# Performance work log

Hardware: AMD Instinct MI355X
Metric: run time of the kernel (lower is better)

Reference implementation:

```python
import jax, jax.numpy as jnp
import numpy as np

D_MODEL = 64
N_RULES = 4
C_DIM = 128
B, T = 32, 8192
LN_EPS = 1e-5
POSSIBLE_STEPS = np.array([2.0, 3.0, 4.0, 5.0, 6.0, 7.0, 8.0], dtype=np.float32)


def setup_inputs() -> dict:
    key = jax.random.key(0)
    ks = jax.random.split(key, 24)
    s = 0.05
    d, h, c = D_MODEL, 2 * D_MODEL, C_DIM
    inp = {
        "cells_state": jax.random.normal(ks[0], (B, T, d), jnp.float32),
        "c_state": jax.random.normal(ks[1], (c,), jnp.float32),
        # n_rules stacked 2-layer rule MLPs: (3d -> 2d, GELU) -> (2d -> d, Tanh)
        "rule_w1": jax.random.normal(ks[2], (N_RULES, 3 * d, h), jnp.float32) * s,
        "rule_b1": jnp.zeros((N_RULES, h), jnp.float32),
        "rule_w2": jax.random.normal(ks[3], (N_RULES, h, d), jnp.float32) * s,
        "rule_b2": jnp.zeros((N_RULES, d), jnp.float32),
        # c_selector: c -> 64 -> n_rules
        "sel_w1": jax.random.normal(ks[4], (c, 64), jnp.float32) * s,
        "sel_b1": jnp.zeros((64,), jnp.float32),
        "sel_w2": jax.random.normal(ks[5], (64, N_RULES), jnp.float32) * s,
        "sel_b2": jnp.zeros((N_RULES,), jnp.float32),
        # c_steps_logits: c -> 32 -> 7
        "st_w1": jax.random.normal(ks[6], (c, 32), jnp.float32) * s,
        "st_b1": jnp.zeros((32,), jnp.float32),
        "st_w2": jax.random.normal(ks[7], (32, 7), jnp.float32) * s,
        "st_b2": jnp.zeros((7,), jnp.float32),
        # c_residual: c -> 32 -> 1, Sigmoid
        "res_w1": jax.random.normal(ks[8], (c, 32), jnp.float32) * s,
        "res_b1": jnp.zeros((32,), jnp.float32),
        "res_w2": jax.random.normal(ks[9], (32, 1), jnp.float32) * s,
        "res_b2": jnp.zeros((1,), jnp.float32),
        # LayerNorm affine
        "ln_g": jnp.ones((d,), jnp.float32),
        "ln_b": jnp.zeros((d,), jnp.float32),
    }
    return inp


def _mlp2(x, w1, b1, w2, b2):
    h = jax.nn.gelu(x @ w1 + b1, approximate=False)
    return h @ w2 + b2


def reference(cells_state, c_state, rule_w1, rule_b1, rule_w2, rule_b2,
              sel_w1, sel_b1, sel_w2, sel_b2, st_w1, st_b1, st_w2, st_b2,
              res_w1, res_b1, res_w2, res_b2, ln_g, ln_b):
    # consciousness-derived controls
    rule_weights = jax.nn.softmax(_mlp2(c_state, sel_w1, sel_b1, sel_w2, sel_b2))  # [n_rules]
    steps_weights = jax.nn.softmax(_mlp2(c_state, st_w1, st_b1, st_w2, st_b2))     # [7]
    n_evolve_soft = jnp.sum(steps_weights * jnp.asarray(POSSIBLE_STEPS))
    # host-side step count (matches torch .item() rounding); concrete, not traced
    n_evolve = max(2, min(8, int(float(n_evolve_soft) + 0.5)))
    alpha = 0.1 + 0.8 * jax.nn.sigmoid(_mlp2(c_state, res_w1, res_b1, res_w2, res_b2))[0]

    cells = cells_state
    for _ in range(n_evolve):
        left = jnp.roll(cells, 1, axis=1)
        right = jnp.roll(cells, -1, axis=1)
        rule_input = jnp.concatenate([cells, left, right], axis=-1)            # [B,T,3d]
        h = jax.nn.gelu(jnp.einsum('btk,rkh->rbth', rule_input, rule_w1)
                        + rule_b1[:, None, None, :], approximate=False)        # [r,B,T,2d]
        out = jnp.tanh(jnp.einsum('rbth,rhd->rbtd', h, rule_w2)
                       + rule_b2[:, None, None, :])                            # [r,B,T,d]
        new_cells = jnp.einsum('r,rbtd->btd', rule_weights, out)
        cells = alpha * cells + (1.0 - alpha) * new_cells

    mu = jnp.mean(cells, axis=-1, keepdims=True)
    var = jnp.mean(jnp.square(cells - mu), axis=-1, keepdims=True)
    normed = (cells - mu) * jax.lax.rsqrt(var + LN_EPS) * ln_g + ln_b
    return normed
```

## Files before the change

### kernel.cpp

```cpp
#include <hip/hip_runtime.h>
#include <cmath>

#define D 64
#define HD 128
#define K1 192
#define TT 8192
#define BBATCH 32
#define RULES 4

typedef _Float16 f16x8 __attribute__((ext_vector_type(8)));
typedef _Float16 f16x4 __attribute__((ext_vector_type(4)));
typedef float f32x4 __attribute__((ext_vector_type(4)));

__device__ __forceinline__ float gelu_exact(float x) {
    return 0.5f * x * (1.0f + erff(x * 0.70710678118654752f));
}

__device__ __forceinline__ float fast_rcp(float x) { return __builtin_amdgcn_rcpf(x); }
__device__ __forceinline__ float fast_exp2(float x) { return __builtin_amdgcn_exp2f(x); }

__device__ __forceinline__ float gelu_tanh(float x) {
    float x2 = x * x;
    float t = x * fmaf(x2, -0.10294443f, -2.30220820f);
    return x * fast_rcp(1.0f + fast_exp2(t));
}
__device__ __forceinline__ float fast_tanh(float x) {
    float e = fast_exp2(x * 2.8853900817779268f);
    return 1.0f - 2.0f * fast_rcp(e + 1.0f);
}

__device__ __forceinline__ f16x4 cvt4_rne(float a, float b, float c, float d) {
    f16x4 r;
    r[0] = (_Float16)a; r[1] = (_Float16)b;
    r[2] = (_Float16)c; r[3] = (_Float16)d;
    return r;
}

__global__ __launch_bounds__(256) void prep_control_kernel(
    const float* __restrict__ rule_w1, const float* __restrict__ rule_w2,
    _Float16* __restrict__ w1b, _Float16* __restrict__ w2b,
    const float* __restrict__ c_state,
    const float* __restrict__ sel_w1, const float* __restrict__ sel_b1,
    const float* __restrict__ sel_w2, const float* __restrict__ sel_b2,
    const float* __restrict__ st_w1,  const float* __restrict__ st_b1,
    const float* __restrict__ st_w2,  const float* __restrict__ st_b2,
    const float* __restrict__ res_w1, const float* __restrict__ res_b1,
    const float* __restrict__ res_w2, const float* __restrict__ res_b2,
    float* __restrict__ ctrl)
{
    if (blockIdx.x < 64) {
        int t = blockIdx.x * 256 + threadIdx.x;
        if (t < 12288) {
            int lane = t & 63;
            int x = t >> 6;
            int htile = x & 31;
            int ks = x >> 5;
            int r = htile >> 3;
            int h128 = (htile & 7) * 16 + (lane & 15);
            int kbase = ks * 32 + (lane >> 4) * 8;
            f16x8 v;
#pragma unroll
            for (int j = 0; j < 8; ++j)
                v[j] = (_Float16)rule_w1[((size_t)r * K1 + kbase + j) * HD + h128];
            ((f16x8*)w1b)[(ks * 32 + htile) * 64 + lane] = v;
        } else if (t < 12288 + 4096) {
            int u = t - 12288;
            int lane = u & 63;
            int mt = (u >> 6) & 3;
            int ks2 = (u >> 8) & 3;
            int r = u >> 10;
            int kbase = ks2 * 32 + (lane >> 4) * 8;
            int d = mt * 16 + (lane & 15);
            f16x8 v;
#pragma unroll
            for (int j = 0; j < 8; ++j)
                v[j] = (_Float16)rule_w2[((size_t)r * HD + kbase + j) * D + d];
            ((f16x8*)w2b)[((r * 4 + ks2) * 4 + mt) * 64 + lane] = v;
        }
        return;
    }

    __shared__ float cs[128];
    __shared__ float h1s[64], h2s[32], h3s[32];
    __shared__ float lg[12];
    int l = threadIdx.x;
    if (l < 64) { cs[l] = c_state[l]; cs[l + 64] = c_state[l + 64]; }
    __syncthreads();
    if (l < 64) {
        float a = sel_b1[l];
        for (int k = 0; k < 128; ++k) a += cs[k] * sel_w1[k * 64 + l];
        h1s[l] = gelu_exact(a);
    }
    if (l < 32) {
        float a = st_b1[l];
        for (int k = 0; k < 128; ++k) a += cs[k] * st_w1[k * 32 + l];
        h2s[l] = gelu_exact(a);
        float a2 = res_b1[l];
        for (int k = 0; k < 128; ++k) a2 += cs[k] * res_w1[k * 32 + l];
        h3s[l] = gelu_exact(a2);
    }
    __syncthreads();
    if (l < 4) {
        float a = sel_b2[l];
        for (int j = 0; j < 64; ++j) a += h1s[j] * sel_w2[j * 4 + l];
        lg[l] = a;
    }
    if (l >= 8 && l < 15) {
        int s = l - 8;
        float a = st_b2[s];
        for (int j = 0; j < 32; ++j) a += h2s[j] * st_w2[j * 7 + s];
        lg[4 + s] = a;
    }
    if (l == 32) {
        float a = res_b2[0];
        for (int j = 0; j < 32; ++j) a += h3s[j] * res_w2[j];
        lg[11] = a;
    }
    __syncthreads();
    if (l == 0) {
        float m = fmaxf(fmaxf(lg[0], lg[1]), fmaxf(lg[2], lg[3]));
        float e0 = expf(lg[0] - m), e1 = expf(lg[1] - m);
        float e2 = expf(lg[2] - m), e3 = expf(lg[3] - m);
        float s = e0 + e1 + e2 + e3;
        ctrl[0] = e0 / s; ctrl[1] = e1 / s; ctrl[2] = e2 / s; ctrl[3] = e3 / s;
        float m2 = lg[4];
        for (int i = 1; i < 7; ++i) m2 = fmaxf(m2, lg[4 + i]);
        float ss = 0.f, es[7];
        for (int i = 0; i < 7; ++i) { es[i] = expf(lg[4 + i] - m2); ss += es[i]; }
        float nsoft = 0.f;
        for (int i = 0; i < 7; ++i) nsoft += (es[i] / ss) * (float)(i + 2);
        int n = (int)(nsoft + 0.5f);
        n = n < 2 ? 2 : (n > 8 ? 8 : n);
        float alpha = 0.1f + 0.8f / (1.0f + expf(-lg[11]));
        ctrl[4] = alpha;
        ctrl[5] = (float)n;
    }
}

__device__ __forceinline__ void evolve_tile(
    int tile, const float* __restrict__ src, float* __restrict__ dst,
    const _Float16* __restrict__ w1b, const _Float16* __restrict__ w2b,
    const float* __restrict__ b1, const float* __restrict__ b2,
    const float* __restrict__ ln_g, const float* __restrict__ ln_b,
    float* __restrict__ fin, bool last, float alpha, float beta, float rwr,
    _Float16* cellsL, _Float16 (*arena)[64 * 136])
{
    int b = tile >> 7;
    int t0 = (tile & 127) << 6;
    const float* srcb = src + (size_t)b * TT * D;

    int tid = threadIdx.x;
    for (int idx = tid; idx < 66 * 16; idx += 256) {
        int row = idx >> 4;
        int c4 = (idx & 15) << 2;
        int tok = (t0 - 1 + row) & (TT - 1);
        f32x4 v = *(const f32x4*)(srcb + (size_t)tok * D + c4);
        *(f16x4*)&cellsL[row * 72 + c4] = cvt4_rne(v[0], v[1], v[2], v[3]);
    }
    __syncthreads();

    int wave = tid >> 6;
    int lane = tid & 63;
    int lrow = lane & 15;
    int lgrp = lane >> 4;
    int r = wave;

    const f16x8* w1v = (const f16x8*)w1b;
    const f16x8* w2v = (const f16x8*)w2b;
    _Float16* hb = &arena[wave][0];

    f32x4 acc1[8][4];
#pragma unroll
    for (int ht = 0; ht < 8; ++ht)
#pragma unroll
        for (int nt = 0; nt < 4; ++nt)
            acc1[ht][nt] = (f32x4){0.f, 0.f, 0.f, 0.f};

#pragma unroll
    for (int ks = 0; ks < 6; ++ks) {
        int k0 = ks * 32 + lgrp * 8;
        int seg = k0 >> 6;
        int kk = k0 & 63;
        int drow = (seg == 0) ? 1 : ((seg == 1) ? 0 : 2);
        f16x8 a_[4];
#pragma unroll
        for (int nt = 0; nt < 4; ++nt)
            a_[nt] = *(const f16x8*)&cellsL[(nt * 16 + lrow + drow) * 72 + kk];
#pragma unroll
        for (int ht = 0; ht < 8; ++ht) {
            f16x8 wf = w1v[(ks * 32 + r * 8 + ht) * 64 + lane];
#pragma unroll
            for (int nt = 0; nt < 4; ++nt)
                acc1[ht][nt] = __builtin_amdgcn_mfma_f32_16x16x32_f16(wf, a_[nt], acc1[ht][nt], 0, 0, 0);
        }
    }

#pragma unroll
    for (int ht = 0; ht < 8; ++ht) {
        f32x4 b1v = *(const f32x4*)&b1[r * HD + ht * 16 + lgrp * 4];
#pragma unroll
        for (int nt = 0; nt < 4; ++nt) {
            float g0 = gelu_tanh(acc1[ht][nt][0] + b1v[0]);
            float g1 = gelu_tanh(acc1[ht][nt][1] + b1v[1]);
            float g2 = gelu_tanh(acc1[ht][nt][2] + b1v[2]);
            float g3 = gelu_tanh(acc1[ht][nt][3] + b1v[3]);
            *(f16x4*)&hb[(nt * 16 + lrow) * 136 + ht * 16 + lgrp * 4]
                = cvt4_rne(g0, g1, g2, g3);
        }
    }

    f32x4 acc2[4][4];
#pragma unroll
    for (int mt = 0; mt < 4; ++mt)
#pragma unroll
        for (int nt = 0; nt < 4; ++nt)
            acc2[mt][nt] = (f32x4){0.f, 0.f, 0.f, 0.f};

#pragma unroll
    for (int ks2 = 0; ks2 < 4; ++ks2) {
        f16x8 a2[4];
#pragma unroll
        for (int nt = 0; nt < 4; ++nt)
            a2[nt] = *(const f16x8*)&hb[(nt * 16 + lrow) * 136 + ks2 * 32 + lgrp * 8];
#pragma unroll
        for (int mt = 0; mt < 4; ++mt) {
            f16x8 bw = w2v[((r * 4 + ks2) * 4 + mt) * 64 + lane];
#pragma unroll
            for (int nt = 0; nt < 4; ++nt)
                acc2[mt][nt] = __builtin_amdgcn_mfma_f32_16x16x32_f16(bw, a2[nt], acc2[mt][nt], 0, 0, 0);
        }
    }

    float* mixw = (float*)hb;
#pragma unroll
    for (int mt = 0; mt < 4; ++mt) {
        f32x4 b2v = *(const f32x4*)&b2[r * D + mt * 16 + lgrp * 4];
#pragma unroll
        for (int nt = 0; nt < 4; ++nt) {
            f32x4 o;
#pragma unroll
            for (int q = 0; q < 4; ++q)
                o[q] = rwr * fast_tanh(acc2[mt][nt][q] + b2v[q]);
            *(f32x4*)&mixw[(nt * 16 + lrow) * 68 + mt * 16 + lgrp * 4] = o;
        }
    }

    __syncthreads();

    int tok = tid >> 2;
    int dq = tid & 3;
    const float* ar0 = (const float*)&arena[0][0];
    const float* ar1 = (const float*)&arena[1][0];
    const float* ar2 = (const float*)&arena[2][0];
    const float* ar3 = (const float*)&arena[3][0];
    int mbase = tok * 68 + dq * 16;
    size_t roff = (size_t)b * TT * D + (size_t)(t0 + tok) * D + dq * 16;

    f32x4 ov[4];
    float m0 = 0.f, m1 = 0.f;
#pragma unroll
    for (int j = 0; j < 4; ++j) {
        f32x4 v0 = *(const f32x4*)(ar0 + mbase + j * 4);
        f32x4 v1 = *(const f32x4*)(ar1 + mbase + j * 4);
        f32x4 v2 = *(const f32x4*)(ar2 + mbase + j * 4);
        f32x4 v3 = *(const f32x4*)(ar3 + mbase + j * 4);
        f32x4 s  = *(const f32x4*)(src + roff + j * 4);
#pragma unroll
        for (int q = 0; q < 4; ++q) {
            float v = alpha * s[q] + beta * (v0[q] + v1[q] + v2[q] + v3[q]);
            ov[j][q] = v; m0 += v; m1 += v * v;
        }
    }

    if (!last) {
#pragma unroll
        for (int j = 0; j < 4; ++j)
            *(f32x4*)(dst + roff + j * 4) = ov[j];
    } else {
        m0 += __shfl_xor(m0, 1, 64); m1 += __shfl_xor(m1, 1, 64);
        m0 += __shfl_xor(m0, 2, 64); m1 += __shfl_xor(m1, 2, 64);
        float mu = m0 * (1.0f / 64.0f);
        float inv = rsqrtf(m1 * (1.0f / 64.0f) - mu * mu + 1e-5f);
#pragma unroll
        for (int j = 0; j < 4; ++j) {
            f32x4 g4 = *(const f32x4*)&ln_g[dq * 16 + j * 4];
            f32x4 b4 = *(const f32x4*)&ln_b[dq * 16 + j * 4];
            f32x4 o;
#pragma unroll
            for (int q = 0; q < 4; ++q)
                o[q] = (ov[j][q] - mu) * inv * g4[q] + b4[q];
            *(f32x4*)(fin + roff + j * 4) = o;
        }
    }
}

__global__ __launch_bounds__(256, 2) void evolve_kernel(
    const float* __restrict__ cells, float* __restrict__ bufA,
    float* __restrict__ out, const float* __restrict__ ctrl,
    const _Float16* __restrict__ w1b, const _Float16* __restrict__ w2b,
    const float* __restrict__ b1, const float* __restrict__ b2,
    const float* __restrict__ ln_g, const float* __restrict__ ln_b, int iter)
{
    int n = (int)ctrl[5];
    if (iter >= n) return;
    bool last = (iter == n - 1);

    const float* src = (iter == 0) ? cells
                       : ((((n - 1 - iter) & 1) == 0) ? (const float*)bufA
                                                      : (const float*)out);
    float* dst = (((n - 2 - iter) & 1) == 0) ? bufA : out;

    __shared__ _Float16 cellsL[66 * 72];
    __shared__ __align__(16) _Float16 arena[4][64 * 136];

    float alpha = ctrl[4];
    float rwr = ctrl[threadIdx.x >> 6];
    evolve_tile(blockIdx.x, src, dst, w1b, w2b, b1, b2, ln_g, ln_b,
                out, last, alpha, 1.0f - alpha, rwr, cellsL, arena);
}

extern "C" void kernel_launch(void* const* d_in, const int* in_sizes, int n_in,
                              void* d_out, int out_size, void* d_ws, size_t ws_size,
                              hipStream_t stream) {
    const float* cells   = (const float*)d_in[0];
    const float* c_state = (const float*)d_in[1];
    const float* rule_w1 = (const float*)d_in[2];
    const float* rule_b1 = (const float*)d_in[3];
    const float* rule_w2 = (const float*)d_in[4];
    const float* rule_b2 = (const float*)d_in[5];
    const float* sel_w1  = (const float*)d_in[6];
    const float* sel_b1  = (const float*)d_in[7];
    const float* sel_w2  = (const float*)d_in[8];
    const float* sel_b2  = (const float*)d_in[9];
    const float* st_w1   = (const float*)d_in[10];
    const float* st_b1   = (const float*)d_in[11];
    const float* st_w2   = (const float*)d_in[12];
    const float* st_b2   = (const float*)d_in[13];
    const float* res_w1  = (const float*)d_in[14];
    const float* res_b1  = (const float*)d_in[15];
    const float* res_w2  = (const float*)d_in[16];
    const float* res_b2  = (const float*)d_in[17];
    const float* ln_g    = (const float*)d_in[18];
    const float* ln_b    = (const float*)d_in[19];

    float* out = (float*)d_out;
    char* ws = (char*)d_ws;
    float* ctrl = (float*)ws;
    _Float16* w1b = (_Float16*)(ws + 256);
    _Float16* w2b = (_Float16*)(ws + 256 + 196608);
    float* bufA = (float*)(ws + (512u * 1024u));

    prep_control_kernel<<<65, 256, 0, stream>>>(
        rule_w1, rule_w2, w1b, w2b, c_state,
        sel_w1, sel_b1, sel_w2, sel_b2,
        st_w1, st_b1, st_w2, st_b2,
        res_w1, res_b1, res_w2, res_b2, ctrl);

    for (int i = 0; i < 8; ++i) {
        evolve_kernel<<<4096, 256, 0, stream>>>(cells, bufA, out, ctrl,
                                                w1b, w2b, rule_b1, rule_b2,
                                                ln_g, ln_b, i);
    }
}
```

Before: 592.8 us.

## Split each rule's token tile across two waves using 512-thread blocks

Each block now runs 8 waves instead of 4. The two waves sharing a rule each handle 32 of the 64 tokens, which halves the per-wave accumulator arrays and lets launch bounds ask for 4 blocks per SM. The final mix and LayerNorm phase is remapped to 8 threads per token, with an extra shuffle step in the reduction. Each wave now loads the full weight fragments for half the tokens, so weight traffic per MFMA doubles, and LDS use per block is unchanged, which may cap how many blocks actually fit.

```diff
diff --git a/kernel.cpp b/kernel.cpp
--- a/kernel.cpp
+++ b/kernel.cpp
@@ -137,164 +137,7 @@
     }
 }
 
-__device__ __forceinline__ void evolve_tile(
-    int tile, const float* __restrict__ src, float* __restrict__ dst,
-    const _Float16* __restrict__ w1b, const _Float16* __restrict__ w2b,
-    const float* __restrict__ b1, const float* __restrict__ b2,
-    const float* __restrict__ ln_g, const float* __restrict__ ln_b,
-    float* __restrict__ fin, bool last, float alpha, float beta, float rwr,
-    _Float16* cellsL, _Float16 (*arena)[64 * 136])
-{
-    int b = tile >> 7;
-    int t0 = (tile & 127) << 6;
-    const float* srcb = src + (size_t)b * TT * D;
-
-    int tid = threadIdx.x;
-    for (int idx = tid; idx < 66 * 16; idx += 256) {
-        int row = idx >> 4;
-        int c4 = (idx & 15) << 2;
-        int tok = (t0 - 1 + row) & (TT - 1);
-        f32x4 v = *(const f32x4*)(srcb + (size_t)tok * D + c4);
-        *(f16x4*)&cellsL[row * 72 + c4] = cvt4_rne(v[0], v[1], v[2], v[3]);
-    }
-    __syncthreads();
-
-    int wave = tid >> 6;
-    int lane = tid & 63;
-    int lrow = lane & 15;
-    int lgrp = lane >> 4;
-    int r = wave;
-
-    const f16x8* w1v = (const f16x8*)w1b;
-    const f16x8* w2v = (const f16x8*)w2b;
-    _Float16* hb = &arena[wave][0];
-
-    f32x4 acc1[8][4];
-#pragma unroll
-    for (int ht = 0; ht < 8; ++ht)
-#pragma unroll
-        for (int nt = 0; nt < 4; ++nt)
-            acc1[ht][nt] = (f32x4){0.f, 0.f, 0.f, 0.f};
-
-#pragma unroll
-    for (int ks = 0; ks < 6; ++ks) {
-        int k0 = ks * 32 + lgrp * 8;
-        int seg = k0 >> 6;
-        int kk = k0 & 63;
-        int drow = (seg == 0) ? 1 : ((seg == 1) ? 0 : 2);
-        f16x8 a_[4];
-#pragma unroll
-        for (int nt = 0; nt < 4; ++nt)
-            a_[nt] = *(const f16x8*)&cellsL[(nt * 16 + lrow + drow) * 72 + kk];
-#pragma unroll
-        for (int ht = 0; ht < 8; ++ht) {
-            f16x8 wf = w1v[(ks * 32 + r * 8 + ht) * 64 + lane];
-#pragma unroll
-            for (int nt = 0; nt < 4; ++nt)
-                acc1[ht][nt] = __builtin_amdgcn_mfma_f32_16x16x32_f16(wf, a_[nt], acc1[ht][nt], 0, 0, 0);
-        }
-    }
-
-#pragma unroll
-    for (int ht = 0; ht < 8; ++ht) {
-        f32x4 b1v = *(const f32x4*)&b1[r * HD + ht * 16 + lgrp * 4];
-#pragma unroll
-        for (int nt = 0; nt < 4; ++nt) {
-            float g0 = gelu_tanh(acc1[ht][nt][0] + b1v[0]);
-            float g1 = gelu_tanh(acc1[ht][nt][1] + b1v[1]);
-            float g2 = gelu_tanh(acc1[ht][nt][2] + b1v[2]);
-            float g3 = gelu_tanh(acc1[ht][nt][3] + b1v[3]);
-            *(f16x4*)&hb[(nt * 16 + lrow) * 136 + ht * 16 + lgrp * 4]
-                = cvt4_rne(g0, g1, g2, g3);
-        }
-    }
-
-    f32x4 acc2[4][4];
-#pragma unroll
-    for (int mt = 0; mt < 4; ++mt)
-#pragma unroll
-        for (int nt = 0; nt < 4; ++nt)
-            acc2[mt][nt] = (f32x4){0.f, 0.f, 0.f, 0.f};
-
-#pragma unroll
-    for (int ks2 = 0; ks2 < 4; ++ks2) {
-        f16x8 a2[4];
-#pragma unroll
-        for (int nt = 0; nt < 4; ++nt)
-            a2[nt] = *(const f16x8*)&hb[(nt * 16 + lrow) * 136 + ks2 * 32 + lgrp * 8];
-#pragma unroll
-        for (int mt = 0; mt < 4; ++mt) {
-            f16x8 bw = w2v[((r * 4 + ks2) * 4 + mt) * 64 + lane];
-#pragma unroll
-            for (int nt = 0; nt < 4; ++nt)
-                acc2[mt][nt] = __builtin_amdgcn_mfma_f32_16x16x32_f16(bw, a2[nt], acc2[mt][nt], 0, 0, 0);
-        }
-    }
-
-    float* mixw = (float*)hb;
-#pragma unroll
-    for (int mt = 0; mt < 4; ++mt) {
-        f32x4 b2v = *(const f32x4*)&b2[r * D + mt * 16 + lgrp * 4];
-#pragma unroll
-        for (int nt = 0; nt < 4; ++nt) {
-            f32x4 o;
-#pragma unroll
-            for (int q = 0; q < 4; ++q)
-                o[q] = rwr * fast_tanh(acc2[mt][nt][q] + b2v[q]);
-            *(f32x4*)&mixw[(nt * 16 + lrow) * 68 + mt * 16 + lgrp * 4] = o;
-        }
-    }
-
-    __syncthreads();
-
-    int tok = tid >> 2;
-    int dq = tid & 3;
-    const float* ar0 = (const float*)&arena[0][0];
-    const float* ar1 = (const float*)&arena[1][0];
-    const float* ar2 = (const float*)&arena[2][0];
-    const float* ar3 = (const float*)&arena[3][0];
-    int mbase = tok * 68 + dq * 16;
-    size_t roff = (size_t)b * TT * D + (size_t)(t0 + tok) * D + dq * 16;
-
-    f32x4 ov[4];
-    float m0 = 0.f, m1 = 0.f;
-#pragma unroll
-    for (int j = 0; j < 4; ++j) {
-        f32x4 v0 = *(const f32x4*)(ar0 + mbase + j * 4);
-        f32x4 v1 = *(const f32x4*)(ar1 + mbase + j * 4);
-        f32x4 v2 = *(const f32x4*)(ar2 + mbase + j * 4);
-        f32x4 v3 = *(const f32x4*)(ar3 + mbase + j * 4);
-        f32x4 s  = *(const f32x4*)(src + roff + j * 4);
-#pragma unroll
-        for (int q = 0; q < 4; ++q) {
-            float v = alpha * s[q] + beta * (v0[q] + v1[q] + v2[q] + v3[q]);
-            ov[j][q] = v; m0 += v; m1 += v * v;
-        }
-    }
-
-    if (!last) {
-#pragma unroll
-        for (int j = 0; j < 4; ++j)
-            *(f32x4*)(dst + roff + j * 4) = ov[j];
-    } else {
-        m0 += __shfl_xor(m0, 1, 64); m1 += __shfl_xor(m1, 1, 64);
-        m0 += __shfl_xor(m0, 2, 64); m1 += __shfl_xor(m1, 2, 64);
-        float mu = m0 * (1.0f / 64.0f);
-        float inv = rsqrtf(m1 * (1.0f / 64.0f) - mu * mu + 1e-5f);
-#pragma unroll
-        for (int j = 0; j < 4; ++j) {
-            f32x4 g4 = *(const f32x4*)&ln_g[dq * 16 + j * 4];
-            f32x4 b4 = *(const f32x4*)&ln_b[dq * 16 + j * 4];
-            f32x4 o;
-#pragma unroll
-            for (int q = 0; q < 4; ++q)
-                o[q] = (ov[j][q] - mu) * inv * g4[q] + b4[q];
-            *(f32x4*)(fin + roff + j * 4) = o;
-        }
-    }
-}
-
-__global__ __launch_bounds__(256, 2) void evolve_kernel(
+__global__ __launch_bounds__(512, 4) void evolve_kernel(
     const float* __restrict__ cells, float* __restrict__ bufA,
     float* __restrict__ out, const float* __restrict__ ctrl,
     const _Float16* __restrict__ w1b, const _Float16* __restrict__ w2b,
@@ -303,20 +146,172 @@
 {
     int n = (int)ctrl[5];
     if (iter >= n) return;
-    bool last = (iter == n - 1);
+    const bool last = (iter == n - 1);
 
     const float* src = (iter == 0) ? cells
                        : ((((n - 1 - iter) & 1) == 0) ? (const float*)bufA
                                                       : (const float*)out);
     float* dst = (((n - 2 - iter) & 1) == 0) ? bufA : out;
 
+    float alpha = ctrl[4];
+    float beta = 1.0f - alpha;
+
     __shared__ _Float16 cellsL[66 * 72];
     __shared__ __align__(16) _Float16 arena[4][64 * 136];
 
-    float alpha = ctrl[4];
-    float rwr = ctrl[threadIdx.x >> 6];
-    evolve_tile(blockIdx.x, src, dst, w1b, w2b, b1, b2, ln_g, ln_b,
-                out, last, alpha, 1.0f - alpha, rwr, cellsL, arena);
+    int tile = blockIdx.x;
+    int b = tile >> 7;
+    int t0 = (tile & 127) << 6;
+    const float* srcb = src + (size_t)b * TT * D;
+
+    int tid = threadIdx.x;
+    for (int idx = tid; idx < 66 * 16; idx += 512) {
+        int row = idx >> 4;
+        int c4 = (idx & 15) << 2;
+        int tok = (t0 - 1 + row) & (TT - 1);
+        f32x4 v = *(const f32x4*)(srcb + (size_t)tok * D + c4);
+        *(f16x4*)&cellsL[row * 72 + c4] = cvt4_rne(v[0], v[1], v[2], v[3]);
+    }
+    __syncthreads();
+
+    int wave = tid >> 6;
+    int lane = tid & 63;
+    int lrow = lane & 15;
+    int lgrp = lane >> 4;
+    int r  = wave >> 1;
+    int th = wave & 1;
+    float rwr = ctrl[r];
+
+    const f16x8* w1v = (const f16x8*)w1b;
+    const f16x8* w2v = (const f16x8*)w2b;
+    _Float16* hb = &arena[r][0];
+
+    f32x4 acc1[8][2];
+#pragma unroll
+    for (int ht = 0; ht < 8; ++ht)
+#pragma unroll
+        for (int nt = 0; nt < 2; ++nt)
+            acc1[ht][nt] = (f32x4){0.f, 0.f, 0.f, 0.f};
+
+#pragma unroll
+    for (int ks = 0; ks < 6; ++ks) {
+        int k0 = ks * 32 + lgrp * 8;
+        int seg = k0 >> 6;
+        int kk = k0 & 63;
+        int drow = (seg == 0) ? 1 : ((seg == 1) ? 0 : 2);
+        f16x8 a_[2];
+#pragma unroll
+        for (int nt = 0; nt < 2; ++nt)
+            a_[nt] = *(const f16x8*)
+                &cellsL[(th * 32 + nt * 16 + lrow + drow) * 72 + kk];
+#pragma unroll
+        for (int ht = 0; ht < 8; ++ht) {
+            f16x8 wf = w1v[(ks * 32 + r * 8 + ht) * 64 + lane];
+#pragma unroll
+            for (int nt = 0; nt < 2; ++nt)
+                acc1[ht][nt] = __builtin_amdgcn_mfma_f32_16x16x32_f16(wf, a_[nt], acc1[ht][nt], 0, 0, 0);
+        }
+    }
+
+#pragma unroll
+    for (int ht = 0; ht < 8; ++ht) {
+        f32x4 b1v = *(const f32x4*)&b1[r * HD + ht * 16 + lgrp * 4];
+#pragma unroll
+        for (int nt = 0; nt < 2; ++nt) {
+            float g0 = gelu_tanh(acc1[ht][nt][0] + b1v[0]);
+            float g1 = gelu_tanh(acc1[ht][nt][1] + b1v[1]);
+            float g2 = gelu_tanh(acc1[ht][nt][2] + b1v[2]);
+            float g3 = gelu_tanh(acc1[ht][nt][3] + b1v[3]);
+            *(f16x4*)&hb[(th * 32 + nt * 16 + lrow) * 136 + ht * 16 + lgrp * 4]
+                = cvt4_rne(g0, g1, g2, g3);
+        }
+    }
+
+    f32x4 acc2[4][2];
+#pragma unroll
+    for (int mt = 0; mt < 4; ++mt)
+#pragma unroll
+        for (int nt = 0; nt < 2; ++nt)
+            acc2[mt][nt] = (f32x4){0.f, 0.f, 0.f, 0.f};
+
+#pragma unroll
+    for (int ks2 = 0; ks2 < 4; ++ks2) {
+        f16x8 a2[2];
+#pragma unroll
+        for (int nt = 0; nt < 2; ++nt)
+            a2[nt] = *(const f16x8*)
+                &hb[(th * 32 + nt * 16 + lrow) * 136 + ks2 * 32 + lgrp * 8];
+#pragma unroll
+        for (int mt = 0; mt < 4; ++mt) {
+            f16x8 bw = w2v[((r * 4 + ks2) * 4 + mt) * 64 + lane];
+#pragma unroll
+            for (int nt = 0; nt < 2; ++nt)
+                acc2[mt][nt] = __builtin_amdgcn_mfma_f32_16x16x32_f16(bw, a2[nt], acc2[mt][nt], 0, 0, 0);
+        }
+    }
+
+    float* mixw = (float*)hb;
+#pragma unroll
+    for (int mt = 0; mt < 4; ++mt) {
+        f32x4 b2v = *(const f32x4*)&b2[r * D + mt * 16 + lgrp * 4];
+#pragma unroll
+        for (int nt = 0; nt < 2; ++nt) {
+            f32x4 o;
+#pragma unroll
+            for (int q = 0; q < 4; ++q)
+                o[q] = rwr * fast_tanh(acc2[mt][nt][q] + b2v[q]);
+            *(f32x4*)&mixw[(th * 32 + nt * 16 + lrow) * 68 + mt * 16 + lgrp * 4] = o;
+        }
+    }
+
+    __syncthreads();
+
+    int tok = tid >> 3;
+    int dq = tid & 7;
+    const float* ar0 = (const float*)&arena[0][0];
+    const float* ar1 = (const float*)&arena[1][0];
+    const float* ar2 = (const float*)&arena[2][0];
+    const float* ar3 = (const float*)&arena[3][0];
+    int mbase = tok * 68 + dq * 8;
+    size_t roff = (size_t)b * TT * D + (size_t)(t0 + tok) * D + dq * 8;
+
+    f32x4 ov[2];
+    float m0 = 0.f, m1 = 0.f;
+#pragma unroll
+    for (int j = 0; j < 2; ++j) {
+        f32x4 v0 = *(const f32x4*)(ar0 + mbase + j * 4);
+        f32x4 v1 = *(const f32x4*)(ar1 + mbase + j * 4);
+        f32x4 v2 = *(const f32x4*)(ar2 + mbase + j * 4);
+        f32x4 v3 = *(const f32x4*)(ar3 + mbase + j * 4);
+        f32x4 s  = *(const f32x4*)(src + roff + j * 4);
+#pragma unroll
+        for (int q = 0; q < 4; ++q) {
+            float v = alpha * s[q] + beta * (v0[q] + v1[q] + v2[q] + v3[q]);
+            ov[j][q] = v; m0 += v; m1 += v * v;
+        }
+    }
+
+    if (!last) {
+#pragma unroll
+        for (int j = 0; j < 2; ++j)
+            *(f32x4*)(dst + roff + j * 4) = ov[j];
+    } else {
+        m0 += __shfl_xor(m0, 1, 64); m1 += __shfl_xor(m1, 1, 64);
+        m0 += __shfl_xor(m0, 2, 64); m1 += __shfl_xor(m1, 2, 64);
+        m0 += __shfl_xor(m0, 4, 64); m1 += __shfl_xor(m1, 4, 64);
+        float mu = m0 * (1.0f / 64.0f);
+        float inv = rsqrtf(m1 * (1.0f / 64.0f) - mu * mu + 1e-5f);
+#pragma unroll
+        for (int j = 0; j < 2; ++j) {
+            f32x4 g4 = *(const f32x4*)&ln_g[dq * 8 + j * 4];
+            f32x4 b4 = *(const f32x4*)&ln_b[dq * 8 + j * 4];
+            f32x4 o;
+#pragma unroll
+            for (int q = 0; q < 4; ++q)
+                o[q] = (ov[j][q] - mu) * inv * g4[q] + b4[q];
+            *(f32x4*)(out + roff + j * 4) = o;
+        }
+    }
 }
 
 extern "C" void kernel_launch(void* const* d_in, const int* in_sizes, int n_in,
@@ -357,7 +352,7 @@
         res_w1, res_b1, res_w2, res_b2, ctrl);
 
     for (int i = 0; i < 8; ++i) {
-        evolve_kernel<<<4096, 256, 0, stream>>>(cells, bufA, out, ctrl,
+        evolve_kernel<<<4096, 512, 0, stream>>>(cells, bufA, out, ctrl,
                                                 w1b, w2b, rule_b1, rule_b2,
                                                 ln_g, ln_b, i);
     }
```

New measurement: 773.6 us. 30.5% more time.
